# Kernel tuning notes

Measured on AMD Instinct MI355X. Metric: run time of the kernel, lower is better.

Reference implementation:

```python
import jax, jax.numpy as jnp
import numpy as np

B, N = 8, 65536
REG_WEIGHT = 1.0


def box2corners(box):
    # box: (B,N,5) [x,y,w,h,alpha] -> corners (B,N,4,2), CCW order
    x, y, w, h, alpha = (box[..., i] for i in range(5))
    x4 = jnp.asarray([0.5, -0.5, -0.5, 0.5], box.dtype) * w[..., None]
    y4 = jnp.asarray([0.5, 0.5, -0.5, -0.5], box.dtype) * h[..., None]
    c = jnp.cos(alpha)[..., None]
    s = jnp.sin(alpha)[..., None]
    cx = x4 * c - y4 * s + x[..., None]
    cy = x4 * s + y4 * c + y[..., None]
    return jnp.stack([cx, cy], axis=-1)


def box_intersection(c1, c2):
    # all 4x4 edge-pair intersections -> pts (B,N,16,2), mask (B,N,16)
    p1, q1 = c1, jnp.roll(c1, -1, axis=2)
    p2, q2 = c2, jnp.roll(c2, -1, axis=2)
    x1, y1 = p1[..., :, None, 0], p1[..., :, None, 1]
    x2, y2 = q1[..., :, None, 0], q1[..., :, None, 1]
    x3, y3 = p2[..., None, :, 0], p2[..., None, :, 1]
    x4, y4 = q2[..., None, :, 0], q2[..., None, :, 1]
    den = (x4 - x3) * (y1 - y2) - (x1 - x2) * (y4 - y3)
    num_t = (y4 - y3) * (x1 - x3) - (x4 - x3) * (y1 - y3)
    num_u = (y1 - y2) * (x1 - x3) - (x1 - x2) * (y1 - y3)
    safe = jnp.where(den == 0, 1.0, den)
    t = jnp.where(den == 0, -1.0, num_t / safe)
    u = jnp.where(den == 0, -1.0, -num_u / safe)
    mask = (t > 0) & (t < 1) & (u > 0) & (u < 1)
    pts = jnp.stack([x1 + t * (x2 - x1), y1 + t * (y2 - y1)], axis=-1)
    pts = pts * mask[..., None]
    Bb, Nn = c1.shape[0], c1.shape[1]
    return pts.reshape(Bb, Nn, 16, 2), mask.reshape(Bb, Nn, 16)


def box1_in_box2(c1, c2):
    # corners of box1 (B,N,4,2) inside box2 via projection on its edges
    a, b, d = c2[..., 0:1, :], c2[..., 1:2, :], c2[..., 3:4, :]
    ab, ad, ap = b - a, d - a, c1 - a
    pab = jnp.sum(ap * ab, -1) / jnp.sum(ab * ab, -1)
    pad_ = jnp.sum(ap * ad, -1) / jnp.sum(ad * ad, -1)
    eps = 1e-6
    return (pab > -eps) & (pab < 1 + eps) & (pad_ > -eps) & (pad_ < 1 + eps)


def oriented_box_intersection_2d(c1, c2):
    pts, m_i = box_intersection(c1, c2)
    m1 = box1_in_box2(c1, c2)
    m2 = box1_in_box2(c2, c1)
    verts = jnp.concatenate([c1, c2, pts], axis=2)   # (B,N,24,2)
    mask = jnp.concatenate([m1, m2, m_i], axis=2)    # (B,N,24)
    mf = mask[..., None].astype(verts.dtype)
    nv = jnp.maximum(jnp.sum(mf, axis=2, keepdims=True), 1.0)
    mean = jnp.sum(verts * mf, axis=2, keepdims=True) / nv  # (B,N,1,2)
    dxy = verts - mean
    ang = jnp.where(mask, jnp.arctan2(dxy[..., 1], dxy[..., 0]), 1e9)
    order = jnp.argsort(ang, axis=-1)
    sv = jnp.take_along_axis(verts, order[..., None], axis=2)
    sm = jnp.take_along_axis(mask, order, axis=-1)
    # pad invalid slots with the first (smallest-angle) valid vertex -> zero shoelace contribution
    poly = jnp.where(sm[..., None], sv, sv[..., 0:1, :])
    x, y = poly[..., 0], poly[..., 1]
    area = 0.5 * jnp.abs(jnp.sum(x * jnp.roll(y, -1, axis=-1) - jnp.roll(x, -1, axis=-1) * y, axis=-1))
    return area, poly


def diff_iou_rotated_3d(box3d1, box3d2, mode='iou'):
    idx = jnp.asarray([0, 1, 3, 4, 6])
    c1 = box2corners(box3d1[..., idx])
    c2 = box2corners(box3d2[..., idx])
    inter_2d, _ = oriented_box_intersection_2d(c1, c2)
    zmax1 = box3d1[..., 2] + 0.5 * box3d1[..., 5]
    zmin1 = box3d1[..., 2] - 0.5 * box3d1[..., 5]
    zmax2 = box3d2[..., 2] + 0.5 * box3d2[..., 5]
    zmin2 = box3d2[..., 2] - 0.5 * box3d2[..., 5]
    z_overlap = jnp.clip(jnp.minimum(zmax1, zmax2) - jnp.maximum(zmin1, zmin2), 0.0)
    inter_3d = inter_2d * z_overlap
    vol1 = box3d1[..., 3] * box3d1[..., 4] * box3d1[..., 5]
    vol2 = box3d2[..., 3] * box3d2[..., 4] * box3d2[..., 5]
    union = vol1 + vol2 - inter_3d
    iou = inter_3d / union
    if mode == 'iou':
        return iou
    inter_diag = jnp.sum((box3d1[..., 0:3] - box3d2[..., 0:3]) ** 2, axis=-1)
    outer_h = jnp.clip(jnp.maximum(zmax1, zmax2) - jnp.minimum(zmin1, zmin2), 0.0)
    out_max = jnp.maximum(c1[:, :, 2], c2[:, :, 2])
    out_min = jnp.minimum(c1[:, :, 0], c2[:, :, 0])
    outer = jnp.clip(out_max - out_min, 0.0)
    outer_diag = outer[..., 0] ** 2 + outer[..., 1] ** 2 + outer_h ** 2
    return jnp.clip(iou - inter_diag / outer_diag, -1.0, 1.0)


def setup_inputs() -> dict:
    key = jax.random.key(0)
    ks = jax.random.split(key, 5)
    ctr = jax.random.uniform(ks[0], (B, N, 3), minval=-50.0, maxval=50.0)
    dims = jax.random.uniform(ks[1], (B, N, 3), minval=1.0, maxval=5.0)
    ang = jax.random.uniform(ks[2], (B, N, 1), minval=-np.pi, maxval=np.pi)
    pred_boxes = jnp.concatenate([ctr, dims, ang], axis=-1)  # (B,N,7)
    noise = jax.random.normal(ks[3], (B, N, 7)) * jnp.asarray([0.5, 0.5, 0.3, 0.3, 0.3, 0.3, 0.2])
    gt7 = pred_boxes + noise
    gt_dims = jnp.maximum(gt7[..., 3:6], 0.1)
    gt_boxes = jnp.concatenate([gt7[..., :3], gt_dims, jnp.sin(gt7[..., 6:7]), jnp.cos(gt7[..., 6:7])], axis=-1)  # (B,N,8)
    pred_iou = jax.random.uniform(ks[4], (B, N)) * 2.0 - 1.0
    mask = jnp.ones((B, N), dtype=bool)
    return {'pred_iou': pred_iou, 'pred_boxes': pred_boxes, 'gt_boxes': gt_boxes, 'mask': mask}


def reference(pred_iou, pred_boxes, gt_boxes, mask):
    mf = mask.astype(pred_iou.dtype).reshape(-1)
    cnt = jnp.maximum(jnp.sum(mf), 1e-4)
    Bb, Nn = pred_iou.shape
    pb = pred_boxes.reshape(1, Bb * Nn, 7)
    gb = gt_boxes.reshape(1, Bb * Nn, 8)
    ang = jnp.arctan2(gb[..., 6:7], gb[..., 7:8])
    gb7 = jnp.concatenate([gb[..., :6], ang], axis=-1)
    target = diff_iou_rotated_3d(pb, gb7, 'iou').reshape(-1) * 2.0 - 1.0
    iou_loss = jnp.sum(jnp.abs(pred_iou.reshape(-1) - target) * mf) / cnt
    diou = diff_iou_rotated_3d(pb, gb7, 'diou').reshape(-1)
    reg_loss = jnp.sum((1.0 - diou) * mf) / cnt
    return iou_loss + reg_loss * REG_WEIGHT
```

## Files before the change

### kernel.cpp

```cpp
#include <hip/hip_runtime.h>


#define RCPF(x) __builtin_amdgcn_rcpf(x)

struct EIn {
    float b[7];
    float g[8];
    float pred;
    float mf;
};

__device__ __forceinline__ void load_elem(EIn& e,
    const float* __restrict__ pred_iou, const float* __restrict__ pred_boxes,
    const float* __restrict__ gt_boxes, const int* __restrict__ mask,
    int gid, bool active)
{
    const float* pb = pred_boxes + (size_t)gid * 7;
    #pragma unroll
    for (int k = 0; k < 7; ++k) e.b[k] = pb[k];
    const float* gb = gt_boxes + (size_t)gid * 8;
    #pragma unroll
    for (int k = 0; k < 8; ++k) e.g[k] = gb[k];
    e.pred = pred_iou[gid];
    e.mf = (active && mask[gid] != 0) ? 1.0f : 0.0f;
}

__device__ __forceinline__ float elem_body(const EIn& e, float* __restrict__ sl)
{
    const float b1x = e.b[0], b1y = e.b[1], b1z = e.b[2];
    const float b1w = e.b[3], b1h = e.b[4], b1l = e.b[5], a1 = e.b[6];
    const float b2x = e.g[0], b2y = e.g[1], b2z = e.g[2];
    const float b2w = e.g[3], b2h = e.g[4], b2l = e.g[5];
    const float gsn = e.g[6], gcs = e.g[7];

    float sn1, cs1;
    __sincosf(a1, &sn1, &cs1);
    const float rn = __builtin_amdgcn_rsqf(gsn * gsn + gcs * gcs);
    const float sn2 = gsn * rn, cs2 = gcs * rn;

    const float xs[4] = {0.5f, -0.5f, -0.5f, 0.5f};
    const float ys[4] = {0.5f, 0.5f, -0.5f, -0.5f};
    float c1x[4], c1y[4], c2x[4], c2y[4];
    #pragma unroll
    for (int k = 0; k < 4; ++k) {
        float xx = xs[k] * b1w, yy = ys[k] * b1h;
        c1x[k] = xx * cs1 - yy * sn1 + b1x;
        c1y[k] = xx * sn1 + yy * cs1 + b1y;
        float x2 = xs[k] * b2w, y2 = ys[k] * b2h;
        c2x[k] = x2 * cs2 - y2 * sn2 + b2x;
        c2y[k] = x2 * sn2 + y2 * cs2 + b2y;
    }

    float2* slot = reinterpret_cast<float2*>(sl);
    unsigned r = 0u;

    const float eps = 1e-6f;

    {
        float ax = c2x[0], ay = c2y[0];
        float abx = c2x[1] - ax, aby = c2y[1] - ay;
        float adx = c2x[3] - ax, ady = c2y[3] - ay;
        float ab2 = abx * abx + aby * aby;
        float ad2 = adx * adx + ady * ady;
        float lo_ab = -eps * ab2, hi_ab = (1.0f + eps) * ab2;
        float lo_ad = -eps * ad2, hi_ad = (1.0f + eps) * ad2;
        #pragma unroll
        for (int k = 0; k < 4; ++k) {
            float apx = c1x[k] - ax, apy = c1y[k] - ay;
            float dab = apx * abx + apy * aby;
            float dad = apx * adx + apy * ady;
            bool ok = (dab > lo_ab) && (dab < hi_ab) && (dad > lo_ad) && (dad < hi_ad);
            unsigned rm = r < 8u ? r : 8u;
            slot[rm] = make_float2(c1x[k], c1y[k]);
            r += ok ? 1u : 0u;
        }
    }
    {
        float ax = c1x[0], ay = c1y[0];
        float abx = c1x[1] - ax, aby = c1y[1] - ay;
        float adx = c1x[3] - ax, ady = c1y[3] - ay;
        float ab2 = abx * abx + aby * aby;
        float ad2 = adx * adx + ady * ady;
        float lo_ab = -eps * ab2, hi_ab = (1.0f + eps) * ab2;
        float lo_ad = -eps * ad2, hi_ad = (1.0f + eps) * ad2;
        #pragma unroll
        for (int k = 0; k < 4; ++k) {
            float apx = c2x[k] - ax, apy = c2y[k] - ay;
            float dab = apx * abx + apy * aby;
            float dad = apx * adx + apy * ady;
            bool ok = (dab > lo_ab) && (dab < hi_ab) && (dad > lo_ad) && (dad < hi_ad);
            unsigned rm = r < 8u ? r : 8u;
            slot[rm] = make_float2(c2x[k], c2y[k]);
            r += ok ? 1u : 0u;
        }
    }

    float e1dx[4], e1dy[4], e2dx[4], e2dy[4];
    #pragma unroll
    for (int l = 0; l < 4; ++l) {
        e1dx[l] = c1x[l] - c1x[(l + 1) & 3];
        e1dy[l] = c1y[l] - c1y[(l + 1) & 3];
        e2dx[l] = c2x[l] - c2x[(l + 1) & 3];
        e2dy[l] = c2y[l] - c2y[(l + 1) & 3];
    }
    #pragma unroll
    for (int l = 0; l < 4; ++l) {
        float x1 = c1x[l], y1 = c1y[l];
        #pragma unroll
        for (int m = 0; m < 4; ++m) {
            float rx = x1 - c2x[m], ry = y1 - c2y[m];
            float den  = e1dx[l] * e2dy[m] - e2dx[m] * e1dy[l];
            float numt = e2dx[m] * ry - e2dy[m] * rx;
            float numu = e1dx[l] * ry - e1dy[l] * rx;
            float aden = fabsf(den);
            bool ok = (numt * den > 0.0f) && (fabsf(numt) < aden) &&
                      (numu * den > 0.0f) && (fabsf(numu) < aden);
            float t = numt * RCPF(den);
            float X = x1 - t * e1dx[l];
            float Y = y1 - t * e1dy[l];
            unsigned rm = r < 8u ? r : 8u;
            slot[rm] = make_float2(X, Y);
            r += ok ? 1u : 0u;
        }
    }

    float px[8], py[8];
    #pragma unroll
    for (int j = 0; j < 8; ++j) {
        float2 p = slot[j];
        px[j] = p.x; py[j] = p.y;
    }
    int kcnt = (int)(r < 8u ? r : 8u);

    float sxm = 0.0f, sym = 0.0f;
    #pragma unroll
    for (int j = 0; j < 8; ++j) {
        bool a = (j < kcnt);
        sxm += a ? px[j] : 0.0f;
        sym += a ? py[j] : 0.0f;
    }
    float rnv = RCPF(fmaxf((float)kcnt, 1.0f));
    float mx = sxm * rnv, my = sym * rnv;

    float key[8];
    #pragma unroll
    for (int j = 0; j < 8; ++j) {
        float dx = px[j] - mx, dy = py[j] - my;
        float ad = fabsf(dx) + fabsf(dy);
        float rr = dx * RCPF(fmaxf(ad, 1e-30f));
        float k = __builtin_copysignf(1.0f - rr, dy);
        key[j] = (j < kcnt) ? k : 1e9f;
    }

    #pragma unroll
    for (int kk = 2; kk <= 8; kk <<= 1) {
        #pragma unroll
        for (int j = kk >> 1; j > 0; j >>= 1) {
            #pragma unroll
            for (int t0 = 0; t0 < 8; ++t0) {
                int o = t0 ^ j;
                if (o > t0) {
                    bool up = (t0 & kk) == 0;
                    float ka = key[t0], kb = key[o];
                    bool sw = up ? (ka > kb) : (ka < kb);
                    float xa = px[t0], xb = px[o];
                    float ya = py[t0], yb = py[o];
                    key[t0] = sw ? kb : ka; key[o] = sw ? ka : kb;
                    px[t0]  = sw ? xb : xa; px[o]  = sw ? xa : xb;
                    py[t0]  = sw ? yb : ya; py[o]  = sw ? ya : yb;
                }
            }
        }
    }

    float x0 = px[0], y0 = py[0];
    float area2 = 0.0f;
    #pragma unroll
    for (int v = 0; v < 8; ++v) {
        bool active = (v < kcnt);
        bool wrap = (v + 1 == kcnt);
        float nx2 = (v == 7) ? x0 : (wrap ? x0 : px[v + 1]);
        float ny2 = (v == 7) ? y0 : (wrap ? y0 : py[v + 1]);
        float term = px[v] * ny2 - nx2 * py[v];
        area2 += active ? term : 0.0f;
    }
    float inter2d = 0.5f * fabsf(area2);

    float zmax1 = b1z + 0.5f * b1l, zmin1 = b1z - 0.5f * b1l;
    float zmax2 = b2z + 0.5f * b2l, zmin2 = b2z - 0.5f * b2l;
    float zov = fmaxf(fminf(zmax1, zmax2) - fmaxf(zmin1, zmin2), 0.0f);
    float inter3d = inter2d * zov;
    float vol1 = b1w * b1h * b1l;
    float vol2 = b2w * b2h * b2l;
    float uni = vol1 + vol2 - inter3d;
    float iou = inter3d * RCPF(uni);
    float target = iou * 2.0f - 1.0f;

    float ddx = b1x - b2x, ddy = b1y - b2y, ddz = b1z - b2z;
    float interdiag = ddx * ddx + ddy * ddy + ddz * ddz;
    float outerh = fmaxf(fmaxf(zmax1, zmax2) - fminf(zmin1, zmin2), 0.0f);
    float omx = fmaxf(fmaxf(c1x[2], c2x[2]) - fminf(c1x[0], c2x[0]), 0.0f);
    float omy = fmaxf(fmaxf(c1y[2], c2y[2]) - fminf(c1y[0], c2y[0]), 0.0f);
    float outerdiag = omx * omx + omy * omy + outerh * outerh;
    float diou = iou - interdiag * RCPF(outerdiag);
    diou = fminf(fmaxf(diou, -1.0f), 1.0f);

    return (fabsf(e.pred - target) + (1.0f - diou)) * e.mf;
}

__global__ __launch_bounds__(256, 4) void iou3d_loss_kernel(
    const float* __restrict__ pred_iou,
    const float* __restrict__ pred_boxes,
    const float* __restrict__ gt_boxes,
    const int*   __restrict__ mask,
    float* __restrict__ sums,
    int M)
{
    __shared__ float lds[256 * 38];
    float* sl0 = &lds[threadIdx.x * 38u];
    float* sl1 = sl0 + 18;

    const int idx0 = blockIdx.x * blockDim.x + threadIdx.x;
    const int stride = gridDim.x * blockDim.x;
    const int idx1 = idx0 + stride;
    const int mlast = M - 1;
    const int i0 = idx0 < M ? idx0 : mlast;
    const int i1 = idx1 < M ? idx1 : mlast;

    EIn e0, e1;
    load_elem(e0, pred_iou, pred_boxes, gt_boxes, mask, i0, idx0 < M);
    load_elem(e1, pred_iou, pred_boxes, gt_boxes, mask, i1, idx1 < M);
    float contrib = elem_body(e0, sl0) + elem_body(e1, sl1);
    float mfv = e0.mf + e1.mf;

    #pragma unroll
    for (int off = 32; off > 0; off >>= 1) {
        contrib += __shfl_down(contrib, off, 64);
        mfv     += __shfl_down(mfv, off, 64);
    }
    __shared__ float sC[4], sM[4];
    const int lane = threadIdx.x & 63;
    const int wv = threadIdx.x >> 6;
    if (lane == 0) { sC[wv] = contrib; sM[wv] = mfv; }
    __syncthreads();
    if (threadIdx.x == 0) {
        float tc = sC[0] + sC[1] + sC[2] + sC[3];
        float tm = sM[0] + sM[1] + sM[2] + sM[3];
        atomicAdd(&sums[0], tc);
        atomicAdd(&sums[1], tm);
    }
}

__global__ void finalize_kernel(const float* __restrict__ sums, float* __restrict__ out) {
    if (threadIdx.x == 0 && blockIdx.x == 0)
        out[0] = sums[0] / fmaxf(sums[1], 1e-4f);
}

extern "C" void kernel_launch(void* const* d_in, const int* in_sizes, int n_in,
                              void* d_out, int out_size, void* d_ws, size_t ws_size,
                              hipStream_t stream) {
    const float* pred_iou   = (const float*)d_in[0];
    const float* pred_boxes = (const float*)d_in[1];
    const float* gt_boxes   = (const float*)d_in[2];
    const int*   mask       = (const int*)d_in[3];
    float* out  = (float*)d_out;
    float* sums = (float*)d_ws;
    const int M = in_sizes[0];

    hipMemsetAsync(sums, 0, 2 * sizeof(float), stream);
    const int block = 256;
    const int elems_per_thread = 2;
    int grid = (M + block * elems_per_thread - 1) / (block * elems_per_thread);
    if (grid < 1) grid = 1;
    hipLaunchKernelGGL(iou3d_loss_kernel, dim3(grid), dim3(block), 0, stream,
                       pred_iou, pred_boxes, gt_boxes, mask, sums, M);
    hipLaunchKernelGGL(finalize_kernel, dim3(1), dim3(64), 0, stream, sums, out);
}
```

Measured before the change: 112.1 us.

## Sort packed index keys with optimal network and use SoA LDS layout

Replaces the bitonic sort that swapped key, x and y triples with a 19-comparator optimal sorting network over unsigned keys. Each key packs the float sort key, converted to an order-preserving integer, with the vertex index in its low 3 bits, so the sorted coordinates are gathered back from LDS afterwards. The LDS scratch moves from per-thread interleaved float2 slots to a structure-of-arrays layout with stride 256 to avoid bank conflicts. The gt_boxes rows are now loaded as float4 vectors. Truncating the low key bits can slightly change the ordering of nearly equal angles.

```diff
diff --git a/kernel.cpp b/kernel.cpp
--- a/kernel.cpp
+++ b/kernel.cpp
@@ -2,6 +2,11 @@
 
 
 #define RCPF(x) __builtin_amdgcn_rcpf(x)
+
+__device__ __forceinline__ unsigned sortKey(float f) {
+    unsigned u = __float_as_uint(f);
+    return (u & 0x80000000u) ? ~u : (u | 0x80000000u);
+}
 
 struct EIn {
     float b[7];
@@ -18,14 +23,16 @@
     const float* pb = pred_boxes + (size_t)gid * 7;
     #pragma unroll
     for (int k = 0; k < 7; ++k) e.b[k] = pb[k];
-    const float* gb = gt_boxes + (size_t)gid * 8;
-    #pragma unroll
-    for (int k = 0; k < 8; ++k) e.g[k] = gb[k];
+    const float4 g0 = reinterpret_cast<const float4*>(gt_boxes)[(size_t)gid * 2 + 0];
+    const float4 g1 = reinterpret_cast<const float4*>(gt_boxes)[(size_t)gid * 2 + 1];
+    e.g[0] = g0.x; e.g[1] = g0.y; e.g[2] = g0.z; e.g[3] = g0.w;
+    e.g[4] = g1.x; e.g[5] = g1.y; e.g[6] = g1.z; e.g[7] = g1.w;
     e.pred = pred_iou[gid];
     e.mf = (active && mask[gid] != 0) ? 1.0f : 0.0f;
 }
 
-__device__ __forceinline__ float elem_body(const EIn& e, float* __restrict__ sl)
+__device__ __forceinline__ float elem_body(const EIn& e,
+    float* __restrict__ X, float* __restrict__ Y)
 {
     const float b1x = e.b[0], b1y = e.b[1], b1z = e.b[2];
     const float b1w = e.b[3], b1h = e.b[4], b1l = e.b[5], a1 = e.b[6];
@@ -51,9 +58,7 @@
         c2y[k] = x2 * sn2 + y2 * cs2 + b2y;
     }
 
-    float2* slot = reinterpret_cast<float2*>(sl);
     unsigned r = 0u;
-
     const float eps = 1e-6f;
 
     {
@@ -71,7 +76,8 @@
             float dad = apx * adx + apy * ady;
             bool ok = (dab > lo_ab) && (dab < hi_ab) && (dad > lo_ad) && (dad < hi_ad);
             unsigned rm = r < 8u ? r : 8u;
-            slot[rm] = make_float2(c1x[k], c1y[k]);
+            X[rm * 256] = c1x[k];
+            Y[rm * 256] = c1y[k];
             r += ok ? 1u : 0u;
         }
     }
@@ -90,11 +96,11 @@
             float dad = apx * adx + apy * ady;
             bool ok = (dab > lo_ab) && (dab < hi_ab) && (dad > lo_ad) && (dad < hi_ad);
             unsigned rm = r < 8u ? r : 8u;
-            slot[rm] = make_float2(c2x[k], c2y[k]);
+            X[rm * 256] = c2x[k];
+            Y[rm * 256] = c2y[k];
             r += ok ? 1u : 0u;
         }
     }
-
     float e1dx[4], e1dy[4], e2dx[4], e2dy[4];
     #pragma unroll
     for (int l = 0; l < 4; ++l) {
@@ -116,10 +122,11 @@
             bool ok = (numt * den > 0.0f) && (fabsf(numt) < aden) &&
                       (numu * den > 0.0f) && (fabsf(numu) < aden);
             float t = numt * RCPF(den);
-            float X = x1 - t * e1dx[l];
-            float Y = y1 - t * e1dy[l];
+            float Xc = x1 - t * e1dx[l];
+            float Yc = y1 - t * e1dy[l];
             unsigned rm = r < 8u ? r : 8u;
-            slot[rm] = make_float2(X, Y);
+            X[rm * 256] = Xc;
+            Y[rm * 256] = Yc;
             r += ok ? 1u : 0u;
         }
     }
@@ -127,8 +134,8 @@
     float px[8], py[8];
     #pragma unroll
     for (int j = 0; j < 8; ++j) {
-        float2 p = slot[j];
-        px[j] = p.x; py[j] = p.y;
+        px[j] = X[j * 256];
+        py[j] = Y[j * 256];
     }
     int kcnt = (int)(r < 8u ? r : 8u);
 
@@ -142,47 +149,46 @@
     float rnv = RCPF(fmaxf((float)kcnt, 1.0f));
     float mx = sxm * rnv, my = sym * rnv;
 
-    float key[8];
+    unsigned key[8];
     #pragma unroll
     for (int j = 0; j < 8; ++j) {
         float dx = px[j] - mx, dy = py[j] - my;
         float ad = fabsf(dx) + fabsf(dy);
         float rr = dx * RCPF(fmaxf(ad, 1e-30f));
         float k = __builtin_copysignf(1.0f - rr, dy);
-        key[j] = (j < kcnt) ? k : 1e9f;
-    }
-
-    #pragma unroll
-    for (int kk = 2; kk <= 8; kk <<= 1) {
-        #pragma unroll
-        for (int j = kk >> 1; j > 0; j >>= 1) {
-            #pragma unroll
-            for (int t0 = 0; t0 < 8; ++t0) {
-                int o = t0 ^ j;
-                if (o > t0) {
-                    bool up = (t0 & kk) == 0;
-                    float ka = key[t0], kb = key[o];
-                    bool sw = up ? (ka > kb) : (ka < kb);
-                    float xa = px[t0], xb = px[o];
-                    float ya = py[t0], yb = py[o];
-                    key[t0] = sw ? kb : ka; key[o] = sw ? ka : kb;
-                    px[t0]  = sw ? xb : xa; px[o]  = sw ? xa : xb;
-                    py[t0]  = sw ? yb : ya; py[o]  = sw ? ya : yb;
-                }
-            }
-        }
-    }
-
-    float x0 = px[0], y0 = py[0];
+        float kf = (j < kcnt) ? k : 1e9f;
+        key[j] = (sortKey(kf) & 0xFFFFFFF8u) | (unsigned)j;
+    }
+
+    #define CE(a, b) { unsigned lo = min(key[a], key[b]); \
+                       unsigned hi = max(key[a], key[b]); \
+                       key[a] = lo; key[b] = hi; }
+    CE(0,1) CE(2,3) CE(4,5) CE(6,7)
+    CE(0,2) CE(1,3) CE(4,6) CE(5,7)
+    CE(1,2) CE(5,6)
+    CE(0,4) CE(1,5) CE(2,6) CE(3,7)
+    CE(2,4) CE(3,5)
+    CE(1,2) CE(3,4) CE(5,6)
+    #undef CE
+
+    float sx[8], sy[8];
+    #pragma unroll
+    for (int j = 0; j < 8; ++j) {
+        unsigned idx = key[j] & 7u;
+        sx[j] = X[idx * 256];
+        sy[j] = Y[idx * 256];
+    }
+
+    float x0 = sx[0], y0 = sy[0];
     float area2 = 0.0f;
     #pragma unroll
     for (int v = 0; v < 8; ++v) {
-        bool active = (v < kcnt);
+        bool act = (v < kcnt);
         bool wrap = (v + 1 == kcnt);
-        float nx2 = (v == 7) ? x0 : (wrap ? x0 : px[v + 1]);
-        float ny2 = (v == 7) ? y0 : (wrap ? y0 : py[v + 1]);
-        float term = px[v] * ny2 - nx2 * py[v];
-        area2 += active ? term : 0.0f;
+        float nx2 = (v == 7) ? x0 : (wrap ? x0 : sx[v + 1]);
+        float ny2 = (v == 7) ? y0 : (wrap ? y0 : sy[v + 1]);
+        float term = sx[v] * ny2 - nx2 * sy[v];
+        area2 += act ? term : 0.0f;
     }
     float inter2d = 0.5f * fabsf(area2);
 
@@ -216,9 +222,12 @@
     float* __restrict__ sums,
     int M)
 {
-    __shared__ float lds[256 * 38];
-    float* sl0 = &lds[threadIdx.x * 38u];
-    float* sl1 = sl0 + 18;
+    __shared__ float sX[2][9][256];
+    __shared__ float sY[2][9][256];
+    float* X0 = &sX[0][0][threadIdx.x];
+    float* Y0 = &sY[0][0][threadIdx.x];
+    float* X1 = &sX[1][0][threadIdx.x];
+    float* Y1 = &sY[1][0][threadIdx.x];
 
     const int idx0 = blockIdx.x * blockDim.x + threadIdx.x;
     const int stride = gridDim.x * blockDim.x;
@@ -230,7 +239,7 @@
     EIn e0, e1;
     load_elem(e0, pred_iou, pred_boxes, gt_boxes, mask, i0, idx0 < M);
     load_elem(e1, pred_iou, pred_boxes, gt_boxes, mask, i1, idx1 < M);
-    float contrib = elem_body(e0, sl0) + elem_body(e1, sl1);
+    float contrib = elem_body(e0, X0, Y0) + elem_body(e1, X1, Y1);
     float mfv = e0.mf + e1.mf;
 
     #pragma unroll
```

New measurement: 113.5 us. About the same (+1.2%).
